# Kernel optimization log

Hardware: AMD Instinct MI355X
Metric: run time of the kernel (lower is better)

Reference implementation:

```python
import jax, jax.numpy as jnp
import numpy as np

D = 1024

def setup_inputs() -> dict:
    key = jax.random.key(0)
    ks = jax.random.split(key, 12)
    sc_in = 1.0 / np.sqrt(D)
    sc_in2 = 1.0 / np.sqrt(2 * D)
    inp = {
        "X1": jax.random.normal(ks[0], (8, D), dtype=jnp.float32),
        "X2": jax.random.normal(ks[1], (8, 2048, D), dtype=jnp.float32),
        # Linear params: weight stored as [in, out], bias [out]
        "Wq1": jax.random.normal(ks[2], (D, D), dtype=jnp.float32) * sc_in,
        "bq1": jax.random.normal(ks[3], (D,), dtype=jnp.float32) * 0.01,
        "Wq2": jax.random.normal(ks[4], (D, D), dtype=jnp.float32) * sc_in,
        "bq2": jax.random.normal(ks[5], (D,), dtype=jnp.float32) * 0.01,
        "Wk1": jax.random.normal(ks[6], (D, D), dtype=jnp.float32) * sc_in,
        "bk1": jax.random.normal(ks[7], (D,), dtype=jnp.float32) * 0.01,
        "Wk2": jax.random.normal(ks[8], (D, D), dtype=jnp.float32) * sc_in,
        "bk2": jax.random.normal(ks[9], (D,), dtype=jnp.float32) * 0.01,
        "Wv": jax.random.normal(ks[10], (2 * D, D), dtype=jnp.float32) * sc_in2,
        "bv": jax.random.normal(ks[11], (D,), dtype=jnp.float32) * 0.01,
        "alpha": jnp.float32(0.5),
    }
    return inp

def reference(X1, X2, Wq1, bq1, Wq2, bq2, Wk1, bk1, Wk2, bk2, Wv, bv, alpha):
    B, S, Dm = X2.shape
    # broadcast X1 [B, D] -> [B, S, D]
    X1e = jnp.broadcast_to(X1[:, None, :], (B, S, Dm))
    X = jnp.concatenate([X1e, X2], axis=-1)  # [B, S, 2D]
    Q1 = X1e @ Wq1 + bq1
    K1 = X1e @ Wk1 + bk1
    Q2 = X2 @ Wq2 + bq2
    K2 = X2 @ Wk2 + bk2
    V = X @ Wv + bv  # [B, S, D]
    s = 1.0 / jnp.sqrt(jnp.float32(Dm))
    A1 = jnp.einsum('bqd,bkd->bqk', Q1, K1) * s
    A2 = jnp.einsum('bqd,bkd->bqk', Q2, K2) * s
    A = jax.nn.softmax(A2, axis=-1) - alpha * jax.nn.softmax(A1, axis=-1)
    return jnp.einsum('bqk,bkd->bqd', A, V)
```

## Files before the change

kernel.cpp:

```cpp
#include <hip/hip_runtime.h>

typedef unsigned short u16;
typedef unsigned int u32;
typedef __bf16 bf16x8 __attribute__((ext_vector_type(8)));
typedef float f32x4 __attribute__((ext_vector_type(4)));
typedef u16 u16x4 __attribute__((ext_vector_type(4)));
typedef u16 u16x8 __attribute__((ext_vector_type(8)));

#define MFMA16(a,b,c) __builtin_amdgcn_mfma_f32_16x16x32_bf16((a),(b),(c),0,0,0)

__device__ __forceinline__ u16 f2bf(float f) {
  u32 u = __builtin_bit_cast(u32, f);
  u += 0x7fffu + ((u >> 16) & 1u);
  return (u16)(u >> 16);
}
__device__ __forceinline__ float bf2f(u16 h) {
  return __builtin_bit_cast(float, (u32)h << 16);
}

typedef __attribute__((address_space(1))) const void gas_void;
typedef __attribute__((address_space(3))) void las_void;
__device__ __forceinline__ void gld16(const void* g, void* l) {
  __builtin_amdgcn_global_load_lds((gas_void*)g, (las_void*)l, 16, 0, 0);
}

__global__ void init_k(float* __restrict__ p)
{
  const int i = blockIdx.x * 256 + threadIdx.x;
  ((f32x4*)p)[i] = (f32x4){0.f, 0.f, 0.f, 0.f};
}

__global__ void wtrans_k(const float* __restrict__ Wq2, const float* __restrict__ Wk2,
                         const float* __restrict__ Wv, u16* __restrict__ Tq,
                         u16* __restrict__ Tk, u16* __restrict__ Tv)
{
  __shared__ float tile[32][33];
  const float* src; u16* dst;
  if (blockIdx.z == 0)      { src = Wq2;             dst = Tq; }
  else if (blockIdx.z == 1) { src = Wk2;             dst = Tk; }
  else                      { src = Wv + 1024*1024;  dst = Tv; }
  const int k0 = blockIdx.x * 32, n0 = blockIdx.y * 32;
  const int tx = threadIdx.x, ty = threadIdx.y;
#pragma unroll
  for (int j = 0; j < 4; ++j)
    tile[ty + 8*j][tx] = src[(size_t)(k0 + ty + 8*j) * 1024 + n0 + tx];
  __syncthreads();
#pragma unroll
  for (int j = 0; j < 4; ++j)
    dst[(size_t)(n0 + ty + 8*j) * 1024 + k0 + tx] = f2bf(tile[tx][ty + 8*j]);
}

__global__ void x2bf_k(const float* __restrict__ X2, u16* __restrict__ X2b)
{
  const size_t i = ((size_t)blockIdx.x * 256 + threadIdx.x) * 8;
  f32x4 a = *(const f32x4*)(X2 + i);
  f32x4 b = *(const f32x4*)(X2 + i + 4);
  u16x8 o;
#pragma unroll
  for (int j = 0; j < 4; ++j) { o[j] = f2bf(a[j]); o[4+j] = f2bf(b[j]); }
  *(u16x8*)(X2b + i) = o;
}

__global__ void v1bv_k(const float* __restrict__ X1, const float* __restrict__ Wv,
                       const float* __restrict__ bv, float* __restrict__ v1bv)
{
  const int b = blockIdx.y, t = threadIdx.x;
  const int d = blockIdx.x * 64 + (t & 63);
  const int jg = t >> 6;
  float a = 0.f;
#pragma unroll 8
  for (int jj = 0; jj < 256; ++jj) {
    const int j = jg * 256 + jj;
    a = fmaf(X1[b*1024 + j], Wv[(size_t)j * 1024 + d], a);
  }
  __shared__ float red[256];
  red[t] = a;
  __syncthreads();
  if (t < 64)
    v1bv[b*1024 + d] = red[t] + red[t+64] + red[t+128] + red[t+192] + bv[d];
}

__global__ __launch_bounds__(256, 2) void gemm_proj(
    const u16* __restrict__ A, const u16* __restrict__ Bt,
    const float* __restrict__ bias, const float* __restrict__ biasB,
    u16* __restrict__ C, int mode, float* __restrict__ Vsum)
{
  __shared__ __attribute__((aligned(16))) u16 ldsA[128 * 64];
  __shared__ __attribute__((aligned(16))) u16 ldsB[128 * 64];
  const int t = threadIdx.x, lane = t & 63, w = t >> 6;
  const int wr = w >> 1, wc = w & 1, l15 = lane & 15, l4 = lane >> 4;
  const int n0 = blockIdx.x * 128, m0 = blockIdx.y * 128;
  const int ebase = w * 2048 + lane * 8;

  f32x4 acc[4][4];
#pragma unroll
  for (int i = 0; i < 4; ++i)
#pragma unroll
    for (int j = 0; j < 4; ++j) acc[i][j] = (f32x4){0.f, 0.f, 0.f, 0.f};

  for (int kt = 0; kt < 16; ++kt) {
    const int k0 = kt * 64;
    __syncthreads();
#pragma unroll
    for (int i = 0; i < 4; ++i) {
      const int elem = ebase + i * 512;
      const int row = elem >> 6, col = elem & 63;
      gld16(A  + (size_t)(m0 + row) * 1024 + k0 + col, (char*)ldsA + w*4096 + i*1024);
      gld16(Bt + (size_t)(n0 + row) * 1024 + k0 + col, (char*)ldsB + w*4096 + i*1024);
    }
    __syncthreads();
#pragma unroll
    for (int inner = 0; inner < 2; ++inner) {
      bf16x8 af[4], bfr[4];
#pragma unroll
      for (int i = 0; i < 4; ++i)
        af[i] = *(const bf16x8*)&ldsA[(64*wr + 16*i + l15) * 64 + inner*32 + l4*8];
#pragma unroll
      for (int j = 0; j < 4; ++j)
        bfr[j] = *(const bf16x8*)&ldsB[(64*wc + 16*j + l15) * 64 + inner*32 + l4*8];
#pragma unroll
      for (int i = 0; i < 4; ++i)
#pragma unroll
        for (int j = 0; j < 4; ++j)
          acc[i][j] = MFMA16(af[i], bfr[j], acc[i][j]);
    }
  }

  if (mode == 0) {
#pragma unroll
    for (int j = 0; j < 4; ++j) {
      const int gc = n0 + 64*wc + 16*j + l15;
      const float bb = bias[gc];
#pragma unroll
      for (int i = 0; i < 4; ++i) {
        const int gr = m0 + 64*wr + 16*i + l4*4;
#pragma unroll
        for (int r = 0; r < 4; ++r)
          C[(size_t)(gr + r) * 1024 + gc] = f2bf(acc[i][j][r] + bb);
      }
    }
  } else {
    const int b = m0 >> 11;
#pragma unroll
    for (int j = 0; j < 4; ++j) {
      const int gc = n0 + 64*wc + 16*j + l15;
      const float bb = biasB[b*1024 + gc];
      float colsum = 0.f;
#pragma unroll
      for (int i = 0; i < 4; ++i) {
        const int s = (m0 & 2047) + 64*wr + 16*i + l4*4;
        u16x4 pk;
#pragma unroll
        for (int r = 0; r < 4; ++r) {
          const float v = acc[i][j][r] + bb;
          pk[r] = f2bf(v);
          colsum += v;
        }
        *(u16x4*)(C + (size_t)b*1024*2048 + (size_t)gc*2048 + s) = pk;
      }
      colsum += __shfl_xor(colsum, 16);
      colsum += __shfl_xor(colsum, 32);
      if (l4 == 0) atomicAdd(&Vsum[b*1024 + gc], colsum);
    }
  }
}

__global__ __launch_bounds__(256, 2) void gemm_sp(
    const u16* __restrict__ Q2, const u16* __restrict__ K2,
    u16* __restrict__ P, float* __restrict__ rowsum)
{
  __shared__ __attribute__((aligned(16))) u16 ldsA[128 * 64];
  __shared__ __attribute__((aligned(16))) u16 ldsB[128 * 64];
  const int id = blockIdx.x;
  const int b = id & 7, idx = id >> 3;
  const int n0 = (idx & 15) * 128, m0 = (idx >> 4) * 128;
  const int t = threadIdx.x, lane = t & 63, w = t >> 6;
  const int wr = w >> 1, wc = w & 1, l15 = lane & 15, l4 = lane >> 4;
  const u16* Ab = Q2 + (size_t)b * 2048 * 1024;
  const u16* Bb = K2 + (size_t)b * 2048 * 1024;
  u16* Cb = P + (size_t)b * 2048 * 2048;
  const int ebase = w * 2048 + lane * 8;

  f32x4 acc[4][4];
#pragma unroll
  for (int i = 0; i < 4; ++i)
#pragma unroll
    for (int j = 0; j < 4; ++j) acc[i][j] = (f32x4){0.f, 0.f, 0.f, 0.f};

  for (int kt = 0; kt < 16; ++kt) {
    const int k0 = kt * 64;
    __syncthreads();
#pragma unroll
    for (int i = 0; i < 4; ++i) {
      const int elem = ebase + i * 512;
      const int row = elem >> 6, col = elem & 63;
      gld16(Ab + (size_t)(m0 + row) * 1024 + k0 + col, (char*)ldsA + w*4096 + i*1024);
      gld16(Bb + (size_t)(n0 + row) * 1024 + k0 + col, (char*)ldsB + w*4096 + i*1024);
    }
    __syncthreads();
#pragma unroll
    for (int inner = 0; inner < 2; ++inner) {
      bf16x8 af[4], bfr[4];
#pragma unroll
      for (int i = 0; i < 4; ++i)
        af[i] = *(const bf16x8*)&ldsA[(64*wr + 16*i + l15) * 64 + inner*32 + l4*8];
#pragma unroll
      for (int j = 0; j < 4; ++j)
        bfr[j] = *(const bf16x8*)&ldsB[(64*wc + 16*j + l15) * 64 + inner*32 + l4*8];
#pragma unroll
      for (int i = 0; i < 4; ++i)
#pragma unroll
        for (int j = 0; j < 4; ++j)
          acc[i][j] = MFMA16(af[i], bfr[j], acc[i][j]);
    }
  }

  const float scale = 0.03125f;
  float rsum[4][4];
#pragma unroll
  for (int i = 0; i < 4; ++i)
#pragma unroll
    for (int r = 0; r < 4; ++r) rsum[i][r] = 0.f;

#pragma unroll
  for (int j = 0; j < 4; ++j) {
    const int gc = n0 + 64*wc + 16*j + l15;
#pragma unroll
    for (int i = 0; i < 4; ++i) {
      const int gr = m0 + 64*wr + 16*i + l4*4;
#pragma unroll
      for (int r = 0; r < 4; ++r) {
        const float e = __expf(acc[i][j][r] * scale);
        rsum[i][r] += e;
        Cb[(size_t)(gr + r) * 2048 + gc] = f2bf(e);
      }
    }
  }
#pragma unroll
  for (int i = 0; i < 4; ++i)
#pragma unroll
    for (int r = 0; r < 4; ++r) {
      float s = rsum[i][r];
      s += __shfl_xor(s, 1);
      s += __shfl_xor(s, 2);
      s += __shfl_xor(s, 4);
      s += __shfl_xor(s, 8);
      if (l15 == 0) {
        const int gr = m0 + 64*wr + 16*i + l4*4 + r;
        atomicAdd(&rowsum[b*2048 + gr], s);
      }
    }
}

__global__ __launch_bounds__(512, 2) void gemm_pv256(
    const u16* __restrict__ P, const u16* __restrict__ Vt,
    const float* __restrict__ rowsum, const float* __restrict__ Vsum,
    const float* __restrict__ alphaP, float* __restrict__ out)
{
  __shared__ __attribute__((aligned(16))) u16 ldsA[256 * 64];
  __shared__ __attribute__((aligned(16))) u16 ldsB[256 * 64];
  const int id = blockIdx.x;
  const int b = id & 7, idx = id >> 3;
  const int n0 = (idx & 3) * 256, m0 = (idx >> 2) * 256;
  const int t = threadIdx.x, lane = t & 63, w = t >> 6;
  const int wr = w >> 2, wc = w & 3, l15 = lane & 15, l4 = lane >> 4;
  const u16* Ab = P  + (size_t)b * 2048 * 2048;
  const u16* Bb = Vt + (size_t)b * 1024 * 2048;

  f32x4 acc[8][4];
#pragma unroll
  for (int i = 0; i < 8; ++i)
#pragma unroll
    for (int j = 0; j < 4; ++j) acc[i][j] = (f32x4){0.f, 0.f, 0.f, 0.f};

  const int ebase = w * 512 + lane * 8;

  for (int kt = 0; kt < 32; ++kt) {
    const int k0 = kt * 64;
    __syncthreads();
#pragma unroll
    for (int i = 0; i < 4; ++i) {
      const int elem = ebase + i * 4096;
      const int row = elem >> 6, col = elem & 63;
      gld16(Ab + (size_t)(m0 + row) * 2048 + k0 + col, (char*)ldsA + i*8192 + w*1024);
      gld16(Bb + (size_t)(n0 + row) * 2048 + k0 + col, (char*)ldsB + i*8192 + w*1024);
    }
    __syncthreads();
#pragma unroll
    for (int inner = 0; inner < 2; ++inner) {
      bf16x8 af[8], bfr[4];
#pragma unroll
      for (int i = 0; i < 8; ++i)
        af[i] = *(const bf16x8*)&ldsA[(128*wr + 16*i + l15) * 64 + inner*32 + l4*8];
#pragma unroll
      for (int j = 0; j < 4; ++j)
        bfr[j] = *(const bf16x8*)&ldsB[(64*wc + 16*j + l15) * 64 + inner*32 + l4*8];
#pragma unroll
      for (int i = 0; i < 8; ++i)
#pragma unroll
        for (int j = 0; j < 4; ++j)
          acc[i][j] = MFMA16(af[i], bfr[j], acc[i][j]);
    }
  }

  const float aS = alphaP[0] * (1.0f / 2048.0f);
  float ctv[4];
#pragma unroll
  for (int j = 0; j < 4; ++j)
    ctv[j] = aS * Vsum[b*1024 + n0 + 64*wc + 16*j + l15];

#pragma unroll
  for (int i = 0; i < 8; ++i) {
    const int grb = m0 + 128*wr + 16*i + l4*4;
    float li[4];
#pragma unroll
    for (int r = 0; r < 4; ++r) li[r] = 1.0f / rowsum[b*2048 + grb + r];
#pragma unroll
    for (int j = 0; j < 4; ++j) {
      const int gc = n0 + 64*wc + 16*j + l15;
#pragma unroll
      for (int r = 0; r < 4; ++r)
        out[(size_t)(b*2048 + grb + r) * 1024 + gc] = acc[i][j][r] * li[r] - ctv[j];
    }
  }
}

extern "C" void kernel_launch(void* const* d_in, const int* in_sizes, int n_in,
                              void* d_out, int out_size, void* d_ws, size_t ws_size,
                              hipStream_t stream)
{
  const float* X1  = (const float*)d_in[0];
  const float* X2  = (const float*)d_in[1];
  const float* Wq2 = (const float*)d_in[4];
  const float* bq2 = (const float*)d_in[5];
  const float* Wk2 = (const float*)d_in[8];
  const float* bk2 = (const float*)d_in[9];
  const float* Wv  = (const float*)d_in[10];
  const float* bv  = (const float*)d_in[11];
  const float* alpha = (const float*)d_in[12];
  float* out = (float*)d_out;

  char* ws = (char*)d_ws;
  u16* Q2  = (u16*)(ws);
  u16* K2  = (u16*)(ws + 33554432);
  u16* Vt  = (u16*)(ws + 67108864);
  u16* P   = (u16*)(ws + 100663296);
  u16* X2b = (u16*)(ws + 134217728);
  u16* Tq  = (u16*)(ws + 167772160);
  u16* Tk  = (u16*)(ws + 169869312);
  u16* Tv  = (u16*)(ws + 171966464);
  float* v1bv   = (float*)(ws + 174063616);
  float* rowsum = (float*)(ws + 174096384);
  float* Vsum   = (float*)(ws + 174161920);

  init_k<<<24, 256, 0, stream>>>(rowsum);
  wtrans_k<<<dim3(32, 32, 3), dim3(32, 8), 0, stream>>>(Wq2, Wk2, Wv, Tq, Tk, Tv);
  x2bf_k<<<8192, 256, 0, stream>>>(X2, X2b);
  v1bv_k<<<dim3(16, 8), 256, 0, stream>>>(X1, Wv, bv, v1bv);

  gemm_proj<<<dim3(8, 128), 256, 0, stream>>>(X2b, Tq, bq2, nullptr, Q2, 0, nullptr);
  gemm_proj<<<dim3(8, 128), 256, 0, stream>>>(X2b, Tk, bk2, nullptr, K2, 0, nullptr);
  gemm_proj<<<dim3(8, 128), 256, 0, stream>>>(X2b, Tv, nullptr, v1bv, Vt, 1, Vsum);

  gemm_sp<<<2048, 256, 0, stream>>>(Q2, K2, P, rowsum);

  gemm_pv256<<<256, 512, 0, stream>>>(P, Vt, rowsum, Vsum, alpha, out);
}
```

Before: 503.0 us.

## Unify GEMMs into double-buffered 256x256 swizzled-LDS pipelined kernel template

```diff
diff --git a/kernel.cpp b/kernel.cpp
--- a/kernel.cpp
+++ b/kernel.cpp
@@ -80,75 +80,163 @@
     v1bv[b*1024 + d] = red[t] + red[t+64] + red[t+128] + red[t+192] + bv[d];
 }
 
-__global__ __launch_bounds__(256, 2) void gemm_proj(
-    const u16* __restrict__ A, const u16* __restrict__ Bt,
-    const float* __restrict__ bias, const float* __restrict__ biasB,
-    u16* __restrict__ C, int mode, float* __restrict__ Vsum)
-{
-  __shared__ __attribute__((aligned(16))) u16 ldsA[128 * 64];
-  __shared__ __attribute__((aligned(16))) u16 ldsB[128 * 64];
+template<int MODE>
+__global__ __launch_bounds__(512, 2) void g256(
+    const u16* __restrict__ A, const u16* __restrict__ B,
+    const float* __restrict__ fa, const float* __restrict__ fb,
+    float* __restrict__ fm, const float* __restrict__ alphaP,
+    void* __restrict__ Cout, int K)
+{
+  __shared__ u16 lds[65536];
+
+  const int id = blockIdx.x;
+  int b = 0, m0, n0;
+  const u16 *Ab, *Bb;
+  if constexpr (MODE <= 1) {
+    n0 = (id & 3) * 256; m0 = (id >> 2) * 256;
+    Ab = A; Bb = B;
+    if constexpr (MODE == 1) b = m0 >> 11;
+  } else if constexpr (MODE == 2) {
+    b = id & 7; const int idx = id >> 3;
+    n0 = (idx & 7) * 256; m0 = (idx >> 3) * 256;
+    Ab = A + (size_t)b * 2048 * 1024;
+    Bb = B + (size_t)b * 2048 * 1024;
+  } else {
+    b = id & 7; const int idx = id >> 3;
+    n0 = (idx & 3) * 256; m0 = (idx >> 2) * 256;
+    Ab = A + (size_t)b * 2048 * 2048;
+    Bb = B + (size_t)b * 1024 * 2048;
+  }
+
   const int t = threadIdx.x, lane = t & 63, w = t >> 6;
-  const int wr = w >> 1, wc = w & 1, l15 = lane & 15, l4 = lane >> 4;
-  const int n0 = blockIdx.x * 128, m0 = blockIdx.y * 128;
-  const int ebase = w * 2048 + lane * 8;
-
-  f32x4 acc[4][4];
-#pragma unroll
-  for (int i = 0; i < 4; ++i)
+  const int wr = w >> 2, wc = w & 3;
+  const int l15 = lane & 15, l4 = lane >> 4;
+
+  const int srow = t >> 2;
+  const int scolsw = (8 * (t & 3)) ^ ((srow & 6) << 2);
+  const int acolsw = (l4 * 8) ^ ((l15 & 6) << 2);
+  const int arow = (128 * wr + l15) * 32 + acolsw;
+  const int brow = 16384 + (64 * wc + l15) * 32 + acolsw;
+
+  const u16* A0 = Ab + (size_t)(m0 + srow) * K + scolsw;
+  const u16* A1 = A0 + (size_t)128 * K;
+  const u16* B0 = Bb + (size_t)(n0 + srow) * K + scolsw;
+  const u16* B1 = B0 + (size_t)128 * K;
+
+  char* ldsc = (char*)lds;
+  const int wo = w * 1024;
+
+  f32x4 acc[8][4];
+#pragma unroll
+  for (int i = 0; i < 8; ++i)
 #pragma unroll
     for (int j = 0; j < 4; ++j) acc[i][j] = (f32x4){0.f, 0.f, 0.f, 0.f};
 
-  for (int kt = 0; kt < 16; ++kt) {
-    const int k0 = kt * 64;
-    __syncthreads();
-#pragma unroll
-    for (int i = 0; i < 4; ++i) {
-      const int elem = ebase + i * 512;
-      const int row = elem >> 6, col = elem & 63;
-      gld16(A  + (size_t)(m0 + row) * 1024 + k0 + col, (char*)ldsA + w*4096 + i*1024);
-      gld16(Bt + (size_t)(n0 + row) * 1024 + k0 + col, (char*)ldsB + w*4096 + i*1024);
-    }
-    __syncthreads();
-#pragma unroll
-    for (int inner = 0; inner < 2; ++inner) {
-      bf16x8 af[4], bfr[4];
-#pragma unroll
-      for (int i = 0; i < 4; ++i)
-        af[i] = *(const bf16x8*)&ldsA[(64*wr + 16*i + l15) * 64 + inner*32 + l4*8];
-#pragma unroll
-      for (int j = 0; j < 4; ++j)
-        bfr[j] = *(const bf16x8*)&ldsB[(64*wc + 16*j + l15) * 64 + inner*32 + l4*8];
-#pragma unroll
-      for (int i = 0; i < 4; ++i)
-#pragma unroll
-        for (int j = 0; j < 4; ++j)
-          acc[i][j] = MFMA16(af[i], bfr[j], acc[i][j]);
-    }
+  gld16(A0,      ldsc + wo);
+  gld16(A1,      ldsc + 8192 + wo);
+  gld16(B0,      ldsc + 32768 + wo);
+  gld16(B1,      ldsc + 40960 + wo);
+  gld16(A0 + 32, ldsc + 16384 + wo);
+  gld16(A1 + 32, ldsc + 24576 + wo);
+  gld16(B0 + 32, ldsc + 49152 + wo);
+  gld16(B1 + 32, ldsc + 57344 + wo);
+  asm volatile("s_waitcnt vmcnt(4)" ::: "memory");
+  __builtin_amdgcn_s_barrier();
+
+  const int NKT = K >> 6;
+  int cur = 0;
+  for (int kt = 0; kt < NKT; ++kt) {
+    const int nxt = cur ^ 1;
+    const size_t koff = (size_t)(kt + 1) * 64;
+    char* dst = ldsc + nxt * 65536 + wo;
+    const u16* la0 = lds + cur * 32768;
+
+    bf16x8 af[8], p0, p1;
+
+    gld16(A0 + koff, dst);
+    gld16(A1 + koff, dst + 8192);
+    gld16(B0 + koff, dst + 32768);
+    gld16(B1 + koff, dst + 40960);
+#pragma unroll
+    for (int m = 0; m < 8; ++m) af[m] = *(const bf16x8*)(la0 + arow + m * 512);
+    p0 = *(const bf16x8*)(la0 + brow);
+    p1 = *(const bf16x8*)(la0 + brow + 512);
+    __builtin_amdgcn_s_setprio(1);
+#pragma unroll
+    for (int m = 0; m < 8; ++m) {
+      acc[m][0] = MFMA16(af[m], p0, acc[m][0]);
+      acc[m][1] = MFMA16(af[m], p1, acc[m][1]);
+    }
+    __builtin_amdgcn_s_setprio(0);
+
+    gld16(A0 + koff + 32, dst + 16384);
+    gld16(A1 + koff + 32, dst + 24576);
+    gld16(B0 + koff + 32, dst + 49152);
+    gld16(B1 + koff + 32, dst + 57344);
+    p0 = *(const bf16x8*)(la0 + brow + 1024);
+    p1 = *(const bf16x8*)(la0 + brow + 1536);
+    __builtin_amdgcn_s_setprio(1);
+#pragma unroll
+    for (int m = 0; m < 8; ++m) {
+      acc[m][2] = MFMA16(af[m], p0, acc[m][2]);
+      acc[m][3] = MFMA16(af[m], p1, acc[m][3]);
+    }
+    __builtin_amdgcn_s_setprio(0);
+
+    asm volatile("s_waitcnt vmcnt(8)" ::: "memory");
+    __builtin_amdgcn_s_barrier();
+
+#pragma unroll
+    for (int m = 0; m < 8; ++m) af[m] = *(const bf16x8*)(la0 + 8192 + arow + m * 512);
+    p0 = *(const bf16x8*)(la0 + 8192 + brow);
+    p1 = *(const bf16x8*)(la0 + 8192 + brow + 512);
+    __builtin_amdgcn_s_setprio(1);
+#pragma unroll
+    for (int m = 0; m < 8; ++m) {
+      acc[m][0] = MFMA16(af[m], p0, acc[m][0]);
+      acc[m][1] = MFMA16(af[m], p1, acc[m][1]);
+    }
+    __builtin_amdgcn_s_setprio(0);
+
+    p0 = *(const bf16x8*)(la0 + 8192 + brow + 1024);
+    p1 = *(const bf16x8*)(la0 + 8192 + brow + 1536);
+    __builtin_amdgcn_s_setprio(1);
+#pragma unroll
+    for (int m = 0; m < 8; ++m) {
+      acc[m][2] = MFMA16(af[m], p0, acc[m][2]);
+      acc[m][3] = MFMA16(af[m], p1, acc[m][3]);
+    }
+    __builtin_amdgcn_s_setprio(0);
+
+    asm volatile("s_waitcnt vmcnt(4)" ::: "memory");
+    __builtin_amdgcn_s_barrier();
+    cur = nxt;
   }
 
-  if (mode == 0) {
+  if constexpr (MODE == 0) {
+    u16* C = (u16*)Cout;
 #pragma unroll
     for (int j = 0; j < 4; ++j) {
       const int gc = n0 + 64*wc + 16*j + l15;
-      const float bb = bias[gc];
-#pragma unroll
-      for (int i = 0; i < 4; ++i) {
-        const int gr = m0 + 64*wr + 16*i + l4*4;
+      const float bb = fa[gc];
+#pragma unroll
+      for (int i = 0; i < 8; ++i) {
+        const int gr = m0 + 128*wr + 16*i + l4*4;
 #pragma unroll
         for (int r = 0; r < 4; ++r)
           C[(size_t)(gr + r) * 1024 + gc] = f2bf(acc[i][j][r] + bb);
       }
     }
-  } else {
-    const int b = m0 >> 11;
+  } else if constexpr (MODE == 1) {
+    u16* C = (u16*)Cout;
 #pragma unroll
     for (int j = 0; j < 4; ++j) {
       const int gc = n0 + 64*wc + 16*j + l15;
-      const float bb = biasB[b*1024 + gc];
+      const float bb = fa[b*1024 + gc];
       float colsum = 0.f;
 #pragma unroll
-      for (int i = 0; i < 4; ++i) {
-        const int s = (m0 & 2047) + 64*wr + 16*i + l4*4;
+      for (int i = 0; i < 8; ++i) {
+        const int s = (m0 & 2047) + 128*wr + 16*i + l4*4;
         u16x4 pk;
 #pragma unroll
         for (int r = 0; r < 4; ++r) {
@@ -160,167 +248,64 @@
       }
       colsum += __shfl_xor(colsum, 16);
       colsum += __shfl_xor(colsum, 32);
-      if (l4 == 0) atomicAdd(&Vsum[b*1024 + gc], colsum);
-    }
-  }
-}
-
-__global__ __launch_bounds__(256, 2) void gemm_sp(
-    const u16* __restrict__ Q2, const u16* __restrict__ K2,
-    u16* __restrict__ P, float* __restrict__ rowsum)
-{
-  __shared__ __attribute__((aligned(16))) u16 ldsA[128 * 64];
-  __shared__ __attribute__((aligned(16))) u16 ldsB[128 * 64];
-  const int id = blockIdx.x;
-  const int b = id & 7, idx = id >> 3;
-  const int n0 = (idx & 15) * 128, m0 = (idx >> 4) * 128;
-  const int t = threadIdx.x, lane = t & 63, w = t >> 6;
-  const int wr = w >> 1, wc = w & 1, l15 = lane & 15, l4 = lane >> 4;
-  const u16* Ab = Q2 + (size_t)b * 2048 * 1024;
-  const u16* Bb = K2 + (size_t)b * 2048 * 1024;
-  u16* Cb = P + (size_t)b * 2048 * 2048;
-  const int ebase = w * 2048 + lane * 8;
-
-  f32x4 acc[4][4];
-#pragma unroll
-  for (int i = 0; i < 4; ++i)
-#pragma unroll
-    for (int j = 0; j < 4; ++j) acc[i][j] = (f32x4){0.f, 0.f, 0.f, 0.f};
-
-  for (int kt = 0; kt < 16; ++kt) {
-    const int k0 = kt * 64;
-    __syncthreads();
-#pragma unroll
-    for (int i = 0; i < 4; ++i) {
-      const int elem = ebase + i * 512;
-      const int row = elem >> 6, col = elem & 63;
-      gld16(Ab + (size_t)(m0 + row) * 1024 + k0 + col, (char*)ldsA + w*4096 + i*1024);
-      gld16(Bb + (size_t)(n0 + row) * 1024 + k0 + col, (char*)ldsB + w*4096 + i*1024);
-    }
-    __syncthreads();
-#pragma unroll
-    for (int inner = 0; inner < 2; ++inner) {
-      bf16x8 af[4], bfr[4];
-#pragma unroll
-      for (int i = 0; i < 4; ++i)
-        af[i] = *(const bf16x8*)&ldsA[(64*wr + 16*i + l15) * 64 + inner*32 + l4*8];
-#pragma unroll
-      for (int j = 0; j < 4; ++j)
-        bfr[j] = *(const bf16x8*)&ldsB[(64*wc + 16*j + l15) * 64 + inner*32 + l4*8];
-#pragma unroll
-      for (int i = 0; i < 4; ++i)
-#pragma unroll
-        for (int j = 0; j < 4; ++j)
-          acc[i][j] = MFMA16(af[i], bfr[j], acc[i][j]);
-    }
-  }
-
-  const float scale = 0.03125f;
-  float rsum[4][4];
-#pragma unroll
-  for (int i = 0; i < 4; ++i)
-#pragma unroll
-    for (int r = 0; r < 4; ++r) rsum[i][r] = 0.f;
-
-#pragma unroll
-  for (int j = 0; j < 4; ++j) {
-    const int gc = n0 + 64*wc + 16*j + l15;
-#pragma unroll
-    for (int i = 0; i < 4; ++i) {
-      const int gr = m0 + 64*wr + 16*i + l4*4;
-#pragma unroll
-      for (int r = 0; r < 4; ++r) {
-        const float e = __expf(acc[i][j][r] * scale);
-        rsum[i][r] += e;
-        Cb[(size_t)(gr + r) * 2048 + gc] = f2bf(e);
-      }
-    }
-  }
-#pragma unroll
-  for (int i = 0; i < 4; ++i)
-#pragma unroll
-    for (int r = 0; r < 4; ++r) {
-      float s = rsum[i][r];
-      s += __shfl_xor(s, 1);
-      s += __shfl_xor(s, 2);
-      s += __shfl_xor(s, 4);
-      s += __shfl_xor(s, 8);
-      if (l15 == 0) {
-        const int gr = m0 + 64*wr + 16*i + l4*4 + r;
-        atomicAdd(&rowsum[b*2048 + gr], s);
-      }
-    }
-}
-
-__global__ __launch_bounds__(512, 2) void gemm_pv256(
-    const u16* __restrict__ P, const u16* __restrict__ Vt,
-    const float* __restrict__ rowsum, const float* __restrict__ Vsum,
-    const float* __restrict__ alphaP, float* __restrict__ out)
-{
-  __shared__ __attribute__((aligned(16))) u16 ldsA[256 * 64];
-  __shared__ __attribute__((aligned(16))) u16 ldsB[256 * 64];
-  const int id = blockIdx.x;
-  const int b = id & 7, idx = id >> 3;
-  const int n0 = (idx & 3) * 256, m0 = (idx >> 2) * 256;
-  const int t = threadIdx.x, lane = t & 63, w = t >> 6;
-  const int wr = w >> 2, wc = w & 3, l15 = lane & 15, l4 = lane >> 4;
-  const u16* Ab = P  + (size_t)b * 2048 * 2048;
-  const u16* Bb = Vt + (size_t)b * 1024 * 2048;
-
-  f32x4 acc[8][4];
-#pragma unroll
-  for (int i = 0; i < 8; ++i)
-#pragma unroll
-    for (int j = 0; j < 4; ++j) acc[i][j] = (f32x4){0.f, 0.f, 0.f, 0.f};
-
-  const int ebase = w * 512 + lane * 8;
-
-  for (int kt = 0; kt < 32; ++kt) {
-    const int k0 = kt * 64;
-    __syncthreads();
-#pragma unroll
-    for (int i = 0; i < 4; ++i) {
-      const int elem = ebase + i * 4096;
-      const int row = elem >> 6, col = elem & 63;
-      gld16(Ab + (size_t)(m0 + row) * 2048 + k0 + col, (char*)ldsA + i*8192 + w*1024);
-      gld16(Bb + (size_t)(n0 + row) * 2048 + k0 + col, (char*)ldsB + i*8192 + w*1024);
-    }
-    __syncthreads();
-#pragma unroll
-    for (int inner = 0; inner < 2; ++inner) {
-      bf16x8 af[8], bfr[4];
-#pragma unroll
-      for (int i = 0; i < 8; ++i)
-        af[i] = *(const bf16x8*)&ldsA[(128*wr + 16*i + l15) * 64 + inner*32 + l4*8];
-#pragma unroll
-      for (int j = 0; j < 4; ++j)
-        bfr[j] = *(const bf16x8*)&ldsB[(64*wc + 16*j + l15) * 64 + inner*32 + l4*8];
-#pragma unroll
-      for (int i = 0; i < 8; ++i)
-#pragma unroll
-        for (int j = 0; j < 4; ++j)
-          acc[i][j] = MFMA16(af[i], bfr[j], acc[i][j]);
-    }
-  }
-
-  const float aS = alphaP[0] * (1.0f / 2048.0f);
-  float ctv[4];
-#pragma unroll
-  for (int j = 0; j < 4; ++j)
-    ctv[j] = aS * Vsum[b*1024 + n0 + 64*wc + 16*j + l15];
-
-#pragma unroll
-  for (int i = 0; i < 8; ++i) {
-    const int grb = m0 + 128*wr + 16*i + l4*4;
-    float li[4];
-#pragma unroll
-    for (int r = 0; r < 4; ++r) li[r] = 1.0f / rowsum[b*2048 + grb + r];
+      if (l4 == 0) atomicAdd(&fm[b*1024 + gc], colsum);
+    }
+  } else if constexpr (MODE == 2) {
+    u16* Cb = (u16*)Cout + (size_t)b * 2048 * 2048;
+    const float scale = 0.03125f;
+    float rs[8][4];
+#pragma unroll
+    for (int i = 0; i < 8; ++i)
+#pragma unroll
+      for (int r = 0; r < 4; ++r) rs[i][r] = 0.f;
 #pragma unroll
     for (int j = 0; j < 4; ++j) {
       const int gc = n0 + 64*wc + 16*j + l15;
 #pragma unroll
-      for (int r = 0; r < 4; ++r)
-        out[(size_t)(b*2048 + grb + r) * 1024 + gc] = acc[i][j][r] * li[r] - ctv[j];
+      for (int i = 0; i < 8; ++i) {
+        const int gr = m0 + 128*wr + 16*i + l4*4;
+#pragma unroll
+        for (int r = 0; r < 4; ++r) {
+          const float e = __expf(acc[i][j][r] * scale);
+          rs[i][r] += e;
+          Cb[(size_t)(gr + r) * 2048 + gc] = f2bf(e);
+        }
+      }
+    }
+#pragma unroll
+    for (int i = 0; i < 8; ++i)
+#pragma unroll
+      for (int r = 0; r < 4; ++r) {
+        float s = rs[i][r];
+        s += __shfl_xor(s, 1);
+        s += __shfl_xor(s, 2);
+        s += __shfl_xor(s, 4);
+        s += __shfl_xor(s, 8);
+        if (l15 == 0) {
+          const int gr = m0 + 128*wr + 16*i + l4*4 + r;
+          atomicAdd(&fm[b*2048 + gr], s);
+        }
+      }
+  } else {
+    float* out = (float*)Cout;
+    const float aS = alphaP[0] * (1.0f / 2048.0f);
+    float ctv[4];
+#pragma unroll
+    for (int j = 0; j < 4; ++j)
+      ctv[j] = aS * fb[b*1024 + n0 + 64*wc + 16*j + l15];
+#pragma unroll
+    for (int i = 0; i < 8; ++i) {
+      const int grb = m0 + 128*wr + 16*i + l4*4;
+      float li[4];
+#pragma unroll
+      for (int r = 0; r < 4; ++r) li[r] = 1.0f / fa[b*2048 + grb + r];
+#pragma unroll
+      for (int j = 0; j < 4; ++j) {
+        const int gc = n0 + 64*wc + 16*j + l15;
+#pragma unroll
+        for (int r = 0; r < 4; ++r)
+          out[(size_t)(b*2048 + grb + r) * 1024 + gc] = acc[i][j][r] * li[r] - ctv[j];
+      }
     }
   }
 }
@@ -358,11 +343,11 @@
   x2bf_k<<<8192, 256, 0, stream>>>(X2, X2b);
   v1bv_k<<<dim3(16, 8), 256, 0, stream>>>(X1, Wv, bv, v1bv);
 
-  gemm_proj<<<dim3(8, 128), 256, 0, stream>>>(X2b, Tq, bq2, nullptr, Q2, 0, nullptr);
-  gemm_proj<<<dim3(8, 128), 256, 0, stream>>>(X2b, Tk, bk2, nullptr, K2, 0, nullptr);
-  gemm_proj<<<dim3(8, 128), 256, 0, stream>>>(X2b, Tv, nullptr, v1bv, Vt, 1, Vsum);
-
-  gemm_sp<<<2048, 256, 0, stream>>>(Q2, K2, P, rowsum);
-
-  gemm_pv256<<<256, 512, 0, stream>>>(P, Vt, rowsum, Vsum, alpha, out);
-}
+  g256<0><<<256, 512, 0, stream>>>(X2b, Tq, bq2, nullptr, nullptr, nullptr, Q2, 1024);
+  g256<0><<<256, 512, 0, stream>>>(X2b, Tk, bk2, nullptr, nullptr, nullptr, K2, 1024);
+  g256<1><<<256, 512, 0, stream>>>(X2b, Tv, v1bv, nullptr, Vsum, nullptr, Vt, 1024);
+
+  g256<2><<<512, 512, 0, stream>>>(Q2, K2, nullptr, nullptr, rowsum, nullptr, P, 1024);
+
+  g256<3><<<256, 512, 0, stream>>>(P, Vt, rowsum, Vsum, nullptr, alpha, out, 2048);
+}
```

After: 479.8 us. -4.6%, faster.
